# Performance work log

Hardware: AMD Instinct MI355X
Metric: run time of the kernel (lower is better)

The kernel has to match this reference:

```python
import jax, jax.numpy as jnp
import numpy as np

# Module constants (from init_kwargs)
K = 7        # kernel_size
STRIDE = 1
PAD = 3
B, C, W = 16, 128, 8192


def setup_inputs() -> dict:
    key = jax.random.key(0)
    k1, k2 = jax.random.split(key)
    x = jax.random.normal(k1, (B, C, W), dtype=jnp.float32)
    mask = jax.random.randint(k2, (B, C, W), 0, 20) < 19
    return {"x": x, "mask": mask}


def reference(x, mask):
    # zero out masked values, then reflect-pad x and zero-pad mask
    masked_x = jnp.where(mask, x, jnp.zeros_like(x))
    xp = jnp.pad(masked_x, ((0, 0), (0, 0), (PAD, PAD)), mode="reflect")
    mp = jnp.pad(mask.astype(x.dtype), ((0, 0), (0, 0), (PAD, PAD)))

    # unfold: gather sliding windows  (B, C, n_out, K)
    n_out = (xp.shape[-1] - K) // STRIDE + 1
    win_idx = jnp.arange(n_out)[:, None] * STRIDE + jnp.arange(K)[None, :]
    xw = xp[..., win_idx]
    mw = mp[..., win_idx]

    # masked values -> +inf so they sort to the end
    x_masked = jnp.where(mw.astype(bool), xw, jnp.inf)
    x_sorted = jnp.sort(x_masked, axis=-1)

    valid_count = mw.sum(axis=-1)                      # float, matches torch mask.float().sum
    median_idx = jnp.clip((valid_count - 1) // 2, 0).astype(jnp.int32)
    med = jnp.take_along_axis(x_sorted, median_idx[..., None], axis=-1)[..., 0]

    # windows with zero valid entries -> nan
    return jnp.where(jnp.isinf(med), jnp.nan, med)
```

## Files before the change

### kernel.cpp

```cpp
#include <hip/hip_runtime.h>
#include <math.h>

#define WIDTH 8192
#define NROW  2048
#define T4    2048
#define NSLOT (NROW * T4)
#define NBLK  2048
#define NTHR  256
#define SSTEP (NBLK * NTHR)
#define ITERS (NSLOT / SSTEP)

#define CE(a, b) { float _lo = fminf(a, b); float _hi = fmaxf(a, b); (a) = _lo; (b) = _hi; }

#define WINDOW(I, DST) {                                                      \
    const unsigned wb = (bits >> ((I) + 1)) & 0x7Fu;                          \
    const int n = __popc(wb);                                                 \
    float v0 = (wb & 1u)  ? xv[(I) + 1] : INF;                                \
    float v1 = (wb & 2u)  ? xv[(I) + 2] : INF;                                \
    float v2 = (wb & 4u)  ? xv[(I) + 3] : INF;                                \
    float v3 = (wb & 8u)  ? xv[(I) + 4] : INF;                                \
    float v4 = (wb & 16u) ? xv[(I) + 5] : INF;                                \
    float v5 = (wb & 32u) ? xv[(I) + 6] : INF;                                \
    float v6 = (wb & 64u) ? xv[(I) + 7] : INF;                                \
    CE(v0, v1); CE(v2, v3); CE(v4, v5);                          \
    CE(v1, v2); CE(v3, v4); CE(v5, v6);                          \
    CE(v0, v1); CE(v2, v3); CE(v4, v5);                          \
    CE(v1, v2); CE(v3, v4); CE(v5, v6);                          \
    CE(v0, v1); CE(v2, v3); CE(v4, v5);                          \
    CE(v1, v2); CE(v3, v4); CE(v5, v6);                          \
    CE(v0, v1); CE(v2, v3);                         \
    const int k = (n - 1) >> 1;                                               \
    float med = (k == 0) ? v0 : (k == 1) ? v1 : (k == 2) ? v2 : v3;           \
    (DST) = (n == 0) ? __builtin_nanf("") : med; }

#define LOAD_TILE(S, X0, X1, X2, M0, M1, M2) {                                \
    const int _t = (S) & (T4 - 1);                                            \
    X0 = (_t > 0)      ? x4[(S) - 1] : Z4;                                    \
    X1 = x4[(S)];                                                             \
    X2 = (_t < T4 - 1) ? x4[(S) + 1] : Z4;                                    \
    M0 = (_t > 0)      ? m4[(S) - 1] : ZI;                                    \
    M1 = m4[(S)];                                                             \
    M2 = (_t < T4 - 1) ? m4[(S) + 1] : ZI; }

__launch_bounds__(NTHR)
__global__ void mmp_kernel(const float* __restrict__ x,
                           const int* __restrict__ mask,
                           float* __restrict__ out) {
    const float4* x4 = (const float4*)x;
    const int4*   m4 = (const int4*)mask;
    float4*       o4 = (float4*)out;

    const int    sid0 = blockIdx.x * NTHR + threadIdx.x;
    const float4 Z4   = make_float4(0.f, 0.f, 0.f, 0.f);
    const int4   ZI   = make_int4(0, 0, 0, 0);
    const float  INF  = __builtin_inff();

    float4 XA0, XA1, XA2, XB0, XB1, XB2;
    int4   MA0, MA1, MA2, MB0, MB1, MB2;
    LOAD_TILE(sid0,         XA0, XA1, XA2, MA0, MA1, MA2);
    LOAD_TILE(sid0 + SSTEP, XB0, XB1, XB2, MB0, MB1, MB2);

#pragma unroll
    for (int it = 0; it < ITERS; ++it) {
        const int s = sid0 + it * SSTEP;

        float4 XC0 = Z4, XC1 = Z4, XC2 = Z4;
        int4   MC0 = ZI, MC1 = ZI, MC2 = ZI;
        if (it < ITERS - 2) {
            LOAD_TILE(s + 2 * SSTEP, XC0, XC1, XC2, MC0, MC1, MC2);
        }

        const unsigned bits =
            (unsigned)((MA0.x != 0)        | ((MA0.y != 0) << 1) |
                       ((MA0.z != 0) << 2) | ((MA0.w != 0) << 3) |
                       ((MA1.x != 0) << 4) | ((MA1.y != 0) << 5) |
                       ((MA1.z != 0) << 6) | ((MA1.w != 0) << 7) |
                       ((MA2.x != 0) << 8) | ((MA2.y != 0) << 9) |
                       ((MA2.z != 0) <<10) | ((MA2.w != 0) <<11));
        const float xv[12] = { XA0.x, XA0.y, XA0.z, XA0.w,
                               XA1.x, XA1.y, XA1.z, XA1.w,
                               XA2.x, XA2.y, XA2.z, XA2.w };

        float o_0, o_1, o_2, o_3;
        WINDOW(0, o_0);
        WINDOW(1, o_1);
        WINDOW(2, o_2);
        WINDOW(3, o_3);
        o4[s] = make_float4(o_0, o_1, o_2, o_3);

        XA0 = XB0; XA1 = XB1; XA2 = XB2;
        MA0 = MB0; MA1 = MB1; MA2 = MB2;
        XB0 = XC0; XB1 = XC1; XB2 = XC2;
        MB0 = MC0; MB1 = MC1; MB2 = MC2;
    }
}

extern "C" void kernel_launch(void* const* d_in, const int* in_sizes, int n_in,
                              void* d_out, int out_size, void* d_ws, size_t ws_size,
                              hipStream_t stream) {
    const float* x    = (const float*)d_in[0];
    const int*   mask = (const int*)d_in[1];
    float*       outp = (float*)d_out;

    mmp_kernel<<<NBLK, NTHR, 0, stream>>>(x, mask, outp);
}
```

Measured before the change: 46.20 us.

## Replace full odd-even sort with split sort and merge-based order statistics

Each 7-element window is now split into a sorted group of 4 and a sorted group of 3. Order statistics 0-3 are computed directly with min/max merge formulas instead of running a full transposition sort network, which cuts the number of min/max operations per window. Boundary tile loads are made unconditional by clamping the index and masking edge bits with an explicit edge mask, and mask bits are packed with plain shifts, which assumes mask values are exactly 0 or 1. Prefetch depth drops from two tiles to one, lowering register pressure at the cost of less latency hiding.

```diff
diff --git a/kernel.cpp b/kernel.cpp
--- a/kernel.cpp
+++ b/kernel.cpp
@@ -15,32 +15,32 @@
 #define WINDOW(I, DST) {                                                      \
     const unsigned wb = (bits >> ((I) + 1)) & 0x7Fu;                          \
     const int n = __popc(wb);                                                 \
-    float v0 = (wb & 1u)  ? xv[(I) + 1] : INF;                                \
-    float v1 = (wb & 2u)  ? xv[(I) + 2] : INF;                                \
-    float v2 = (wb & 4u)  ? xv[(I) + 3] : INF;                                \
-    float v3 = (wb & 8u)  ? xv[(I) + 4] : INF;                                \
-    float v4 = (wb & 16u) ? xv[(I) + 5] : INF;                                \
-    float v5 = (wb & 32u) ? xv[(I) + 6] : INF;                                \
-    float v6 = (wb & 64u) ? xv[(I) + 7] : INF;                                \
-    CE(v0, v1); CE(v2, v3); CE(v4, v5);                          \
-    CE(v1, v2); CE(v3, v4); CE(v5, v6);                          \
-    CE(v0, v1); CE(v2, v3); CE(v4, v5);                          \
-    CE(v1, v2); CE(v3, v4); CE(v5, v6);                          \
-    CE(v0, v1); CE(v2, v3); CE(v4, v5);                          \
-    CE(v1, v2); CE(v3, v4); CE(v5, v6);                          \
-    CE(v0, v1); CE(v2, v3);                         \
+    float a0 = (wb & 1u)  ? xv[(I) + 1] : INF;                                \
+    float a1 = (wb & 2u)  ? xv[(I) + 2] : INF;                                \
+    float a2 = (wb & 4u)  ? xv[(I) + 3] : INF;                                \
+    float a3 = (wb & 8u)  ? xv[(I) + 4] : INF;                                \
+    float t0 = (wb & 16u) ? xv[(I) + 5] : INF;                                \
+    float t1 = (wb & 32u) ? xv[(I) + 6] : INF;                                \
+    float t2 = (wb & 64u) ? xv[(I) + 7] : INF;                                \
+    CE(a0, a1); CE(a2, a3); CE(a0, a2); CE(a1, a3); CE(a1, a2);    \
+    CE(t0, t1); CE(t1, t2); CE(t0, t1);                            \
+    const float M0 = fminf(a0, t0);                                           \
+    const float M1 = fminf(fminf(a1, t1), fmaxf(a0, t0));                     \
+    const float M2 = fminf(fminf(a2, t2),                                     \
+                           fminf(fmaxf(a1, t0), fmaxf(a0, t1)));              \
+    const float M3 = fminf(fminf(a3, fmaxf(a2, t0)),                          \
+                           fminf(fmaxf(a1, t1), fmaxf(a0, t2)));              \
     const int k = (n - 1) >> 1;                                               \
-    float med = (k == 0) ? v0 : (k == 1) ? v1 : (k == 2) ? v2 : v3;           \
+    float med = (k <= 0) ? M0 : (k == 1) ? M1 : (k == 2) ? M2 : M3;           \
     (DST) = (n == 0) ? __builtin_nanf("") : med; }
 
-#define LOAD_TILE(S, X0, X1, X2, M0, M1, M2) {                                \
-    const int _t = (S) & (T4 - 1);                                            \
-    X0 = (_t > 0)      ? x4[(S) - 1] : Z4;                                    \
-    X1 = x4[(S)];                                                             \
-    X2 = (_t < T4 - 1) ? x4[(S) + 1] : Z4;                                    \
-    M0 = (_t > 0)      ? m4[(S) - 1] : ZI;                                    \
-    M1 = m4[(S)];                                                             \
-    M2 = (_t < T4 - 1) ? m4[(S) + 1] : ZI; }
+#define LOAD_TILE(S, X0, X1, X2, M0, M1, M2, EM) {                            \
+    const int _t  = (S) & (T4 - 1);                                           \
+    const int _sm = (S) - ((_t > 0)      ? 1 : 0);                            \
+    const int _sp = (S) + ((_t < T4 - 1) ? 1 : 0);                            \
+    X0 = x4[_sm];  X1 = x4[(S)];  X2 = x4[_sp];                               \
+    M0 = m4[_sm];  M1 = m4[(S)];  M2 = m4[_sp];                               \
+    EM = ((_t > 0) ? 0xFu : 0u) | 0xF0u | ((_t < T4 - 1) ? 0xF00u : 0u); }
 
 __launch_bounds__(NTHR)
 __global__ void mmp_kernel(const float* __restrict__ x,
@@ -50,33 +50,31 @@
     const int4*   m4 = (const int4*)mask;
     float4*       o4 = (float4*)out;
 
-    const int    sid0 = blockIdx.x * NTHR + threadIdx.x;
-    const float4 Z4   = make_float4(0.f, 0.f, 0.f, 0.f);
-    const int4   ZI   = make_int4(0, 0, 0, 0);
-    const float  INF  = __builtin_inff();
+    const int   sid0 = blockIdx.x * NTHR + threadIdx.x;
+    const float INF  = __builtin_inff();
 
-    float4 XA0, XA1, XA2, XB0, XB1, XB2;
-    int4   MA0, MA1, MA2, MB0, MB1, MB2;
-    LOAD_TILE(sid0,         XA0, XA1, XA2, MA0, MA1, MA2);
-    LOAD_TILE(sid0 + SSTEP, XB0, XB1, XB2, MB0, MB1, MB2);
+    float4 XA0, XA1, XA2; int4 MA0, MA1, MA2; unsigned emA;
+    LOAD_TILE(sid0, XA0, XA1, XA2, MA0, MA1, MA2, emA);
 
 #pragma unroll
     for (int it = 0; it < ITERS; ++it) {
         const int s = sid0 + it * SSTEP;
 
-        float4 XC0 = Z4, XC1 = Z4, XC2 = Z4;
-        int4   MC0 = ZI, MC1 = ZI, MC2 = ZI;
-        if (it < ITERS - 2) {
-            LOAD_TILE(s + 2 * SSTEP, XC0, XC1, XC2, MC0, MC1, MC2);
+        float4 XB0, XB1, XB2; int4 MB0, MB1, MB2; unsigned emB = 0;
+        if (it < ITERS - 1) {
+            LOAD_TILE(s + SSTEP, XB0, XB1, XB2, MB0, MB1, MB2, emB);
+        } else {
+            XB0 = XA0; XB1 = XA1; XB2 = XA2;
+            MB0 = MA0; MB1 = MA1; MB2 = MA2;
         }
 
         const unsigned bits =
-            (unsigned)((MA0.x != 0)        | ((MA0.y != 0) << 1) |
-                       ((MA0.z != 0) << 2) | ((MA0.w != 0) << 3) |
-                       ((MA1.x != 0) << 4) | ((MA1.y != 0) << 5) |
-                       ((MA1.z != 0) << 6) | ((MA1.w != 0) << 7) |
-                       ((MA2.x != 0) << 8) | ((MA2.y != 0) << 9) |
-                       ((MA2.z != 0) <<10) | ((MA2.w != 0) <<11));
+            (((unsigned)MA0.x)       | ((unsigned)MA0.y << 1) |
+             ((unsigned)MA0.z << 2)  | ((unsigned)MA0.w << 3) |
+             ((unsigned)MA1.x << 4)  | ((unsigned)MA1.y << 5) |
+             ((unsigned)MA1.z << 6)  | ((unsigned)MA1.w << 7) |
+             ((unsigned)MA2.x << 8)  | ((unsigned)MA2.y << 9) |
+             ((unsigned)MA2.z << 10) | ((unsigned)MA2.w << 11)) & emA;
         const float xv[12] = { XA0.x, XA0.y, XA0.z, XA0.w,
                                XA1.x, XA1.y, XA1.z, XA1.w,
                                XA2.x, XA2.y, XA2.z, XA2.w };
@@ -90,8 +88,7 @@
 
         XA0 = XB0; XA1 = XB1; XA2 = XB2;
         MA0 = MB0; MA1 = MB1; MA2 = MB2;
-        XB0 = XC0; XB1 = XC1; XB2 = XC2;
-        MB0 = MC0; MB1 = MC1; MB2 = MC2;
+        emA = emB;
     }
 }
 
```

Measured after the change: 41.79 us. -9.6%, faster.
